# Optimization experiments

Measured on AMD Instinct MI355X. Metric: run time of the kernel, lower is better.

The kernel has to match this reference:

```python
import jax, jax.numpy as jnp
import numpy as np

B, T = 8, 1024
C_IN, C_H = 4096, 4096
K_I, K_H = 3, 3
INIT_SPARSITY = 0.15


def _fixed_fanin_bipartite(rng, n_out, n_in, k):
    # exactly k True entries per row, distinct columns
    r = rng.random((n_out, n_in))
    cols = np.argsort(r, axis=1)[:, :k]
    A = np.zeros((n_out, n_in), np.float32)
    np.put_along_axis(A, cols, 1.0, axis=1)
    return A


def _fixed_fanin_graph(rng, n, k):
    # exactly k True entries per row, distinct non-self columns
    r = rng.random((n, n))
    np.fill_diagonal(r, 2.0)  # exclude self-loops
    cols = np.argsort(r, axis=1)[:, :k]
    A = np.zeros((n, n), np.float32)
    np.put_along_axis(A, cols, 1.0, axis=1)
    return A


def setup_inputs() -> dict:
    rng = np.random.default_rng(0)
    z = jnp.asarray(rng.random((B, T, C_IN)) < INIT_SPARSITY)          # bool (B,T,C_in)
    h0 = jnp.asarray(rng.random((B, C_H)) < INIT_SPARSITY)             # bool (B,C_h)
    A_input_f = jnp.asarray(_fixed_fanin_bipartite(rng, C_H, C_IN, K_I))  # (C_h,C_in) f32
    A_hidden_f = jnp.asarray(_fixed_fanin_graph(rng, C_H, K_H))           # (C_h,C_h) f32
    return {"z": z, "h0": h0, "A_input_f": A_input_f, "A_hidden_f": A_hidden_f}


def reference(z, h0, A_input_f, A_hidden_f):
    # AND-of-ORs CA: h_i(t) = [OR over input fan-in of z(t)] AND [OR over hidden fan-in of h(t-1)]
    z_tf = jnp.moveaxis(z, -2, 0)  # (T, B, C_in)

    def step(h, z_t):
        input_or = (z_t.astype(jnp.float32) @ A_input_f.T) > 0   # (B, C_h) bool
        hidden_or = (h.astype(jnp.float32) @ A_hidden_f.T) > 0   # (B, C_h) bool
        h_new = input_or & hidden_or
        return h_new, h_new

    _, h_seq = jax.lax.scan(step, h0, z_tf)   # (T, B, C_h)
    h_seq = jnp.moveaxis(h_seq, 0, -2)        # (B, T, C_h)
    return jnp.concatenate([z, h_seq], axis=-1)  # (B, T, C_in + C_h) bool
```

## Files before the change

### kernel.cpp

```cpp
#include <hip/hip_runtime.h>
#include <stdint.h>

#define B_   8
#define T_   1024
#define CIN_ 4096
#define CH_  4096


__device__ __forceinline__ uint32_t bytes_nonzero01(uint32_t w) {
  uint32_t t = (w & 0x7F7F7F7Fu) + 0x7F7F7F7Fu;
  t = (t | w) & 0x80808080u;
  return t >> 7;
}

__device__ __forceinline__ uint32_t load4(const void* base, long idx4, int es) {
  if (es == 1) {
    uint32_t w = ((const uint32_t*)base)[idx4];
    return bytes_nonzero01(w);
  } else if (es == 2) {
    uint32_t w0 = ((const uint32_t*)base)[idx4 * 2];
    uint32_t w1 = ((const uint32_t*)base)[idx4 * 2 + 1];
    uint32_t r = 0;
    r |= ((w0 & 0xFFFFu) != 0u) ? 0x00000001u : 0u;
    r |= ((w0 >> 16)     != 0u) ? 0x00000100u : 0u;
    r |= ((w1 & 0xFFFFu) != 0u) ? 0x00010000u : 0u;
    r |= ((w1 >> 16)     != 0u) ? 0x01000000u : 0u;
    return r;
  } else {
    uint4 w = ((const uint4*)base)[idx4];
    uint32_t r = 0;
    r |= (w.x != 0u) ? 0x00000001u : 0u;
    r |= (w.y != 0u) ? 0x00000100u : 0u;
    r |= (w.z != 0u) ? 0x00010000u : 0u;
    r |= (w.w != 0u) ? 0x01000000u : 0u;
    return r;
  }
}

__device__ __forceinline__ uint4 expand01(uint32_t v4) {
  uint4 r = { v4 & 1u, (v4 >> 8) & 1u, (v4 >> 16) & 1u, (v4 >> 24) & 1u };
  return r;
}

__global__ __launch_bounds__(256) void extract_kernel(const float* __restrict__ Ain,
                                                      const float* __restrict__ Ah,
                                                      uint32_t* __restrict__ idxin,
                                                      uint32_t* __restrict__ idxh,
                                                      const uint32_t* __restrict__ z,
                                                      uint32_t* __restrict__ modep) {
  if (blockIdx.x == 2048) {
    __shared__ int sB, sH, sW, sL;
    const int n = threadIdx.x;
    if (n == 0) { sB = 1; sH = 1; sW = 1; sL = 0; }
    __syncthreads();
    int okB = 1, okH = 1, okW = 1, low = 0;
    for (int k = 0; k < 16; ++k) {
      uint32_t w = z[n + 256 * k];
      if ((w & 0xFEFEFEFEu) != 0u) okB = 0;
      uint32_t lo = w & 0xFFFFu, hi = w >> 16;
      if (!((lo == 0u || lo == 0x3F80u) && (hi == 0u || hi == 0x3F80u))) okH = 0;
      if (!(w == 0u || w == 1u)) okW = 0;
      if (lo != 0u) low = 1;
    }
    if (!okB) atomicAnd(&sB, 0);
    if (!okH) atomicAnd(&sH, 0);
    if (!okW) atomicAnd(&sW, 0);
    if (low)  atomicOr(&sL, 1);
    __syncthreads();
    if (n == 0) {
      uint32_t mode;
      if (sW)      mode = 4;
      else if (sB) mode = 1;
      else if (sH) mode = sL ? 2 : 4;
      else         mode = 1;
      modep[0] = mode;
    }
    return;
  }
  const int wave = threadIdx.x >> 6;
  const int lane = threadIdx.x & 63;
  const int row  = blockIdx.x * 4 + wave;
  const float* A;
  uint32_t* outp;
  if (row < 4096) { A = Ain + (long)row * 4096;          outp = idxin + row * 3; }
  else            { A = Ah  + (long)(row - 4096) * 4096; outp = idxh + (row - 4096) * 3; }
  __shared__ int cnt[4];
  if (lane == 0) cnt[wave] = 0;
  __syncthreads();
  const float4* A4 = (const float4*)A;
  #pragma unroll
  for (int it = 0; it < 16; ++it) {
    float4 v = A4[it * 64 + lane];
    int cbase = (it * 64 + lane) * 4;
    if (v.x != 0.0f) { int p = atomicAdd(&cnt[wave], 1); if (p < 3) outp[p] = cbase;     }
    if (v.y != 0.0f) { int p = atomicAdd(&cnt[wave], 1); if (p < 3) outp[p] = cbase + 1; }
    if (v.z != 0.0f) { int p = atomicAdd(&cnt[wave], 1); if (p < 3) outp[p] = cbase + 2; }
    if (v.w != 0.0f) { int p = atomicAdd(&cnt[wave], 1); if (p < 3) outp[p] = cbase + 3; }
  }
}

__global__ __launch_bounds__(1024) void inor_kernel(const void* __restrict__ z,
                                                    const uint32_t* __restrict__ idxin,
                                                    const uint32_t* __restrict__ modep,
                                                    uint32_t* __restrict__ in_orb,
                                                    uint32_t* __restrict__ out) {
  const int t = blockIdx.x;
  const int n = threadIdx.x;
  const int es = (int)modep[0];
  __shared__ __align__(16) unsigned char zp[4096];
  uint32_t acc = 0;
  #pragma unroll
  for (int b = 0; b < B_; ++b) {
    uint32_t v4 = load4(z, ((long)b * T_ + t) * 1024 + n, es);
    acc |= v4 << b;
    ((uint4*)(out + ((long)b * T_ + t) * 8192))[n] = expand01(v4);
  }
  ((uint32_t*)zp)[n] = acc;
  __syncthreads();
  const uint4* ip = (const uint4*)(idxin + n * 12);
  uint4 q0 = ip[0], q1 = ip[1], q2 = ip[2];
  uint32_t r0 = (uint32_t)zp[q0.x] | zp[q0.y] | zp[q0.z];
  uint32_t r1 = (uint32_t)zp[q0.w] | zp[q1.x] | zp[q1.y];
  uint32_t r2 = (uint32_t)zp[q1.z] | zp[q1.w] | zp[q2.x];
  uint32_t r3 = (uint32_t)zp[q2.y] | zp[q2.z] | zp[q2.w];
  in_orb[t * 1024 + n] = r0 | (r1 << 8) | (r2 << 16) | (r3 << 24);
}

__global__ __launch_bounds__(1024) void scan_kernel(const uint32_t* __restrict__ in_orb,
                                                    const uint32_t* __restrict__ idxh,
                                                    const void* __restrict__ h0,
                                                    const uint32_t* __restrict__ modep,
                                                    uint32_t* __restrict__ out) {
  const int b = blockIdx.x;
  const int n = threadIdx.x;
  const int es = (int)modep[0];
  __shared__ __align__(16) unsigned char hbuf[2][4096];

  uint32_t d[4][3];
  {
    const uint4* p = (const uint4*)(idxh + n * 12);
    uint4 q0 = p[0], q1 = p[1], q2 = p[2];
    d[0][0] = q0.x; d[0][1] = q0.y; d[0][2] = q0.z;
    d[1][0] = q0.w; d[1][1] = q1.x; d[1][2] = q1.y;
    d[2][0] = q1.z; d[2][1] = q1.w; d[2][2] = q2.x;
    d[3][0] = q2.y; d[3][1] = q2.z; d[3][2] = q2.w;
  }

  ((uint32_t*)hbuf[0])[n] = load4(h0, (long)b * 1024 + n, es);
  __syncthreads();

  uint32_t* outh = out + (long)b * T_ * 8192 + 4096;

  int p = 0;
  uint32_t inw = in_orb[n];
  for (int t = 0; t < T_; ++t) {
    uint32_t inw_next = (t + 1 < T_) ? in_orb[(t + 1) * 1024 + n] : 0u;
    const unsigned char* hc = &hbuf[p][0];
    unsigned char* hn = &hbuf[p ^ 1][0];

    uint32_t mask = (inw >> b) & 0x01010101u;
    uint32_t out4 = 0;
    if (mask) {
      if (mask & 0x00000001u) {
        uint32_t v = (uint32_t)hc[d[0][0]] | hc[d[0][1]] | hc[d[0][2]];
        out4 |= v;
      }
      if (mask & 0x00000100u) {
        uint32_t v = (uint32_t)hc[d[1][0]] | hc[d[1][1]] | hc[d[1][2]];
        out4 |= v << 8;
      }
      if (mask & 0x00010000u) {
        uint32_t v = (uint32_t)hc[d[2][0]] | hc[d[2][1]] | hc[d[2][2]];
        out4 |= v << 16;
      }
      if (mask & 0x01000000u) {
        uint32_t v = (uint32_t)hc[d[3][0]] | hc[d[3][1]] | hc[d[3][2]];
        out4 |= v << 24;
      }
    }
    ((uint32_t*)hn)[n] = out4;
    ((uint4*)(outh + (long)t * 8192))[n] = expand01(out4);
    __syncthreads();

    inw = inw_next;
    p ^= 1;
  }
}

extern "C" void kernel_launch(void* const* d_in, const int* in_sizes, int n_in,
                              void* d_out, int out_size, void* d_ws, size_t ws_size,
                              hipStream_t stream) {
  const void*  z   = d_in[0];
  const void*  h0  = d_in[1];
  const float* Ain = (const float*)d_in[2];
  const float* Ah  = (const float*)d_in[3];
  uint32_t* out = (uint32_t*)d_out;

  char* ws = (char*)d_ws;
  uint32_t* modep = (uint32_t*)(ws);
  uint32_t* idxin = (uint32_t*)(ws + 256);
  uint32_t* idxh  = (uint32_t*)(ws + 256 + 49152);
  uint32_t* inorb = (uint32_t*)(ws + 98560);

  extract_kernel<<<2049, 256,  0, stream>>>(Ain, Ah, idxin, idxh,
                                            (const uint32_t*)z, modep);
  inor_kernel   <<<T_,   1024, 0, stream>>>(z, idxin, modep, inorb, out);
  scan_kernel   <<<B_,   1024, 0, stream>>>(inorb, idxh, h0, modep, out);
}
```

Baseline: 950.4 us.

## Reorder hidden fan-in slots to reduce LDS bank conflicts in scan

Adds a small preprocessing kernel that packs each thread's 12 hidden fan-in indices, tagged with their byte lane, into 16-bit entries. It then swaps slots between threads' slot positions using a per-slot LDS bank histogram to spread the byte gathers across banks. The scan kernel now issues 12 predicated byte gathers in an order where all lanes in a wave hit fewer conflicting banks at the same time. This adds an extra launch and a heuristic swap pass in exchange for fewer LDS conflicts in the serial 1024-step loop.

```diff
diff --git a/kernel.cpp b/kernel.cpp
--- a/kernel.cpp
+++ b/kernel.cpp
@@ -99,6 +99,49 @@
   }
 }
 
+__global__ __launch_bounds__(64) void opt_kernel(const uint32_t* __restrict__ idxh,
+                                                 uint32_t* __restrict__ tbl32) {
+  const int w = blockIdx.x;
+  const int l = threadIdx.x;
+  const int tid = w * 64 + l;
+  __shared__ int hist[12][32];
+  __shared__ uint32_t slt[64][13];
+  #pragma unroll
+  for (int k = 0; k < 4; ++k)
+    #pragma unroll
+    for (int s = 0; s < 3; ++s)
+      slt[l][k * 3 + s] = idxh[(tid * 4 + k) * 3 + s] | (uint32_t)(k << 12);
+  __syncthreads();
+  for (int r = 0; r < 16; ++r) {
+    for (int i = l; i < 384; i += 64) ((int*)hist)[i] = 0;
+    __syncthreads();
+    #pragma unroll
+    for (int s = 0; s < 12; ++s)
+      atomicAdd(&hist[s][(slt[l][s] >> 2) & 31], 1);
+    __syncthreads();
+    if (((l + r) & 1) == 0) {
+      int rr = r % 11;
+      for (int i = 0; i < 6; ++i) {
+        int s1 = (i == 0) ? 11 : (rr + i) % 11;
+        int s2 = (i == 0) ? rr : (rr + 11 - i) % 11;
+        uint32_t t1v = slt[l][s1], t2v = slt[l][s2];
+        int b1 = (int)((t1v >> 2) & 31), b2 = (int)((t2v >> 2) & 31);
+        if (b1 != b2) {
+          int d = -(hist[s1][b1] > 2) + (hist[s2][b1] >= 2)
+                - (hist[s2][b2] > 2) + (hist[s1][b2] >= 2);
+          if (d < 0) { slt[l][s1] = t2v; slt[l][s2] = t1v; }
+        }
+      }
+    }
+    __syncthreads();
+  }
+  #pragma unroll
+  for (int i = 0; i < 6; ++i) {
+    uint32_t t0 = slt[l][2 * i], t1 = slt[l][2 * i + 1];
+    tbl32[tid * 6 + i] = t0 | (t1 << 16);
+  }
+}
+
 __global__ __launch_bounds__(1024) void inor_kernel(const void* __restrict__ z,
                                                     const uint32_t* __restrict__ idxin,
                                                     const uint32_t* __restrict__ modep,
@@ -127,7 +170,7 @@
 }
 
 __global__ __launch_bounds__(1024) void scan_kernel(const uint32_t* __restrict__ in_orb,
-                                                    const uint32_t* __restrict__ idxh,
+                                                    const uint32_t* __restrict__ tbl32,
                                                     const void* __restrict__ h0,
                                                     const uint32_t* __restrict__ modep,
                                                     uint32_t* __restrict__ out) {
@@ -136,14 +179,16 @@
   const int es = (int)modep[0];
   __shared__ __align__(16) unsigned char hbuf[2][4096];
 
-  uint32_t d[4][3];
+  uint32_t tup[12];
   {
-    const uint4* p = (const uint4*)(idxh + n * 12);
-    uint4 q0 = p[0], q1 = p[1], q2 = p[2];
-    d[0][0] = q0.x; d[0][1] = q0.y; d[0][2] = q0.z;
-    d[1][0] = q0.w; d[1][1] = q1.x; d[1][2] = q1.y;
-    d[2][0] = q1.z; d[2][1] = q1.w; d[2][2] = q2.x;
-    d[3][0] = q2.y; d[3][1] = q2.z; d[3][2] = q2.w;
+    const uint2* tp = (const uint2*)(tbl32 + n * 6);
+    uint2 a0 = tp[0], a1 = tp[1], a2 = tp[2];
+    uint32_t wsv[6] = { a0.x, a0.y, a1.x, a1.y, a2.x, a2.y };
+    #pragma unroll
+    for (int i = 0; i < 6; ++i) {
+      tup[2 * i]     = wsv[i] & 0xFFFFu;
+      tup[2 * i + 1] = wsv[i] >> 16;
+    }
   }
 
   ((uint32_t*)hbuf[0])[n] = load4(h0, (long)b * 1024 + n, es);
@@ -160,23 +205,12 @@
 
     uint32_t mask = (inw >> b) & 0x01010101u;
     uint32_t out4 = 0;
-    if (mask) {
-      if (mask & 0x00000001u) {
-        uint32_t v = (uint32_t)hc[d[0][0]] | hc[d[0][1]] | hc[d[0][2]];
-        out4 |= v;
-      }
-      if (mask & 0x00000100u) {
-        uint32_t v = (uint32_t)hc[d[1][0]] | hc[d[1][1]] | hc[d[1][2]];
-        out4 |= v << 8;
-      }
-      if (mask & 0x00010000u) {
-        uint32_t v = (uint32_t)hc[d[2][0]] | hc[d[2][1]] | hc[d[2][2]];
-        out4 |= v << 16;
-      }
-      if (mask & 0x01000000u) {
-        uint32_t v = (uint32_t)hc[d[3][0]] | hc[d[3][1]] | hc[d[3][2]];
-        out4 |= v << 24;
-      }
+    #pragma unroll
+    for (int s = 0; s < 12; ++s) {
+      uint32_t tt = tup[s];
+      uint32_t sh = (tt >> 12) << 3;
+      if ((mask >> sh) & 1u)
+        out4 |= ((uint32_t)hc[tt & 0xFFFu]) << sh;
     }
     ((uint32_t*)hn)[n] = out4;
     ((uint4*)(outh + (long)t * 8192))[n] = expand01(out4);
@@ -201,9 +235,11 @@
   uint32_t* idxin = (uint32_t*)(ws + 256);
   uint32_t* idxh  = (uint32_t*)(ws + 256 + 49152);
   uint32_t* inorb = (uint32_t*)(ws + 98560);
+  uint32_t* tbl32 = (uint32_t*)(ws + 4292864);
 
   extract_kernel<<<2049, 256,  0, stream>>>(Ain, Ah, idxin, idxh,
                                             (const uint32_t*)z, modep);
+  opt_kernel    <<<16,   64,   0, stream>>>(idxh, tbl32);
   inor_kernel   <<<T_,   1024, 0, stream>>>(z, idxin, modep, inorb, out);
-  scan_kernel   <<<B_,   1024, 0, stream>>>(inorb, idxh, h0, modep, out);
-}
+  scan_kernel   <<<B_,   1024, 0, stream>>>(inorb, tbl32, h0, modep, out);
+}
```

After: 1.220 ms. 28.4% more time.
